# Performance work log

Hardware: AMD Instinct MI355X
Metric: run time of the kernel (lower is better)

Reference implementation:

```python
import jax, jax.numpy as jnp
import numpy as np

N_NODES = 100000
N_EDGES = 1600000
D_FEAT = 128


def setup_inputs() -> dict:
    key = jax.random.key(0)
    k1, k2 = jax.random.split(key)
    x = jax.random.normal(k1, (N_NODES, D_FEAT), dtype=jnp.float32)
    edge_index = jax.random.randint(k2, (2, N_EDGES), 0, N_NODES, dtype=jnp.int64)
    return {"x": x, "edge_index": edge_index}


def reference(x, edge_index):
    # gather source/target node features: [E, D] each
    src = x[edge_index[0]]
    dst = x[edge_index[1]]
    # per-edge dot product -> [E], then sigmoid
    dot = jnp.sum(src * dst, axis=-1)
    return jax.nn.sigmoid(dot)
```

## Files before the change

kernel.cpp:

```cpp
#include <hip/hip_runtime.h>
#include <hip/hip_fp16.h>
#include <math.h>

#define D_FEAT 128

__global__ __launch_bounds__(256) void convert_x_fp16_kernel(
    const float* __restrict__ x, __half* __restrict__ xh, int n_elems)
{
    int i = blockIdx.x * blockDim.x + threadIdx.x;
    int base = i * 8;
    if (base >= n_elems) return;
    const float4* p = reinterpret_cast<const float4*>(x + base);
    float4 f0 = p[0];
    float4 f1 = p[1];
    __half2 h[4];
    h[0] = __floats2half2_rn(f0.x, f0.y);
    h[1] = __floats2half2_rn(f0.z, f0.w);
    h[2] = __floats2half2_rn(f1.x, f1.y);
    h[3] = __floats2half2_rn(f1.z, f1.w);
    *reinterpret_cast<float4*>(xh + base) = *reinterpret_cast<float4*>(h);
}

struct alignas(16) h8 { __half2 h[4]; };

__device__ __forceinline__ float dot8(const h8& a, const h8& b) {
    float acc = 0.f;
#pragma unroll
    for (int k = 0; k < 4; ++k) {
        float2 fa = __half22float2(a.h[k]);
        float2 fb = __half22float2(b.h[k]);
        acc += fa.x * fb.x + fa.y * fb.y;
    }
    return acc;
}

__global__ __launch_bounds__(256) void edge_dot_sigmoid_fp16_kernel(
    const __half* __restrict__ xh,
    const int* __restrict__ ei,
    float* __restrict__ out,
    int n_edges)
{
    const int lane = threadIdx.x & 15;
    const int grp  = threadIdx.x >> 4;
    const int base = blockIdx.x * 32;
    const int e0 = base + grp;
    const int e1 = base + 16 + grp;

    if (e0 >= n_edges) return;

    const int s0 = ei[e0];
    const int d0 = ei[n_edges + e0];
    const bool has1 = (e1 < n_edges);
    const int s1 = has1 ? ei[e1] : s0;
    const int d1 = has1 ? ei[n_edges + e1] : d0;

    const h8* ps0 = reinterpret_cast<const h8*>(xh + (size_t)s0 * D_FEAT) + lane;
    const h8* pd0 = reinterpret_cast<const h8*>(xh + (size_t)d0 * D_FEAT) + lane;
    const h8* ps1 = reinterpret_cast<const h8*>(xh + (size_t)s1 * D_FEAT) + lane;
    const h8* pd1 = reinterpret_cast<const h8*>(xh + (size_t)d1 * D_FEAT) + lane;

    h8 a0 = *ps0;
    h8 b0 = *pd0;
    h8 a1 = *ps1;
    h8 b1 = *pd1;

    float acc0 = dot8(a0, b0);
    float acc1 = dot8(a1, b1);

    acc0 += __shfl_xor(acc0, 1, 16);
    acc0 += __shfl_xor(acc0, 2, 16);
    acc0 += __shfl_xor(acc0, 4, 16);
    acc0 += __shfl_xor(acc0, 8, 16);

    acc1 += __shfl_xor(acc1, 1, 16);
    acc1 += __shfl_xor(acc1, 2, 16);
    acc1 += __shfl_xor(acc1, 4, 16);
    acc1 += __shfl_xor(acc1, 8, 16);

    if (lane == 0) {
        out[e0] = 1.0f / (1.0f + __expf(-acc0));
        if (has1) out[e1] = 1.0f / (1.0f + __expf(-acc1));
    }
}

__global__ __launch_bounds__(256) void edge_dot_sigmoid_fp32_kernel(
    const float* __restrict__ x,
    const int* __restrict__ ei,
    float* __restrict__ out,
    int n_edges)
{
    const int lane = threadIdx.x & 15;
    const int e = blockIdx.x * 16 + (threadIdx.x >> 4);
    if (e >= n_edges) return;

    const int s = ei[e];
    const int d = ei[n_edges + e];

    const float4* sp = reinterpret_cast<const float4*>(x + (size_t)s * D_FEAT) + lane * 2;
    const float4* dp = reinterpret_cast<const float4*>(x + (size_t)d * D_FEAT) + lane * 2;

    float4 a0 = sp[0], a1 = sp[1], b0 = dp[0], b1 = dp[1];

    float acc = a0.x * b0.x + a0.y * b0.y + a0.z * b0.z + a0.w * b0.w
              + a1.x * b1.x + a1.y * b1.y + a1.z * b1.z + a1.w * b1.w;

    acc += __shfl_xor(acc, 1, 16);
    acc += __shfl_xor(acc, 2, 16);
    acc += __shfl_xor(acc, 4, 16);
    acc += __shfl_xor(acc, 8, 16);

    if (lane == 0) out[e] = 1.0f / (1.0f + __expf(-acc));
}

extern "C" void kernel_launch(void* const* d_in, const int* in_sizes, int n_in,
                              void* d_out, int out_size, void* d_ws, size_t ws_size,
                              hipStream_t stream) {
    const float* x   = (const float*)d_in[0];
    const int*   ei  = (const int*)d_in[1];
    float*       out = (float*)d_out;

    const int n_x     = in_sizes[0];
    const int n_edges = in_sizes[1] / 2;

    const size_t need = (size_t)n_x * sizeof(__half);
    if (ws_size >= need) {
        __half* xh = (__half*)d_ws;
        int n_chunks = (n_x + 7) / 8;
        convert_x_fp16_kernel<<<(n_chunks + 255) / 256, 256, 0, stream>>>(x, xh, n_x);
        dim3 grid((n_edges + 31) / 32);
        edge_dot_sigmoid_fp16_kernel<<<grid, 256, 0, stream>>>(xh, ei, out, n_edges);
    } else {
        dim3 grid((n_edges + 15) / 16);
        edge_dot_sigmoid_fp32_kernel<<<grid, 256, 0, stream>>>(x, ei, out, n_edges);
    }
}
```

Before: 111.8 us.

## Process eight edges per 16-lane group with shuffled indices and fdot2

Each 16-lane group now handles eight edges instead of two. The lanes load the source and destination indices cooperatively in one coalesced read and broadcast them with shuffles. All sixteen row gathers are issued before any arithmetic, which raises memory-level parallelism. The dot product uses the packed fp16 fdot2 builtin, and the per-edge results are gathered so that eight lanes write eight consecutive outputs. Register use rises to hold sixteen 16-byte vectors per thread, which may lower occupancy, and the grid is four times smaller.

```diff
diff --git a/kernel.cpp b/kernel.cpp
--- a/kernel.cpp
+++ b/kernel.cpp
@@ -3,6 +3,24 @@
 #include <math.h>
 
 #define D_FEAT 128
+
+typedef _Float16 f16x2 __attribute__((ext_vector_type(2)));
+struct alignas(16) h8v { f16x2 h[4]; };
+
+__device__ __forceinline__ float dot8(const h8v& a, const h8v& b, float acc) {
+#if __has_builtin(__builtin_amdgcn_fdot2)
+#pragma unroll
+    for (int k = 0; k < 4; ++k)
+        acc = __builtin_amdgcn_fdot2(a.h[k], b.h[k], acc, false);
+#else
+#pragma unroll
+    for (int k = 0; k < 4; ++k) {
+        acc += (float)a.h[k].x * (float)b.h[k].x;
+        acc += (float)a.h[k].y * (float)b.h[k].y;
+    }
+#endif
+    return acc;
+}
 
 __global__ __launch_bounds__(256) void convert_x_fp16_kernel(
     const float* __restrict__ x, __half* __restrict__ xh, int n_elems)
@@ -21,19 +39,6 @@
     *reinterpret_cast<float4*>(xh + base) = *reinterpret_cast<float4*>(h);
 }
 
-struct alignas(16) h8 { __half2 h[4]; };
-
-__device__ __forceinline__ float dot8(const h8& a, const h8& b) {
-    float acc = 0.f;
-#pragma unroll
-    for (int k = 0; k < 4; ++k) {
-        float2 fa = __half22float2(a.h[k]);
-        float2 fb = __half22float2(b.h[k]);
-        acc += fa.x * fb.x + fa.y * fb.y;
-    }
-    return acc;
-}
-
 __global__ __launch_bounds__(256) void edge_dot_sigmoid_fp16_kernel(
     const __half* __restrict__ xh,
     const int* __restrict__ ei,
@@ -42,44 +47,41 @@
 {
     const int lane = threadIdx.x & 15;
     const int grp  = threadIdx.x >> 4;
-    const int base = blockIdx.x * 32;
-    const int e0 = base + grp;
-    const int e1 = base + 16 + grp;
+    const long eb  = (long)blockIdx.x * 128 + grp * 8;
 
-    if (e0 >= n_edges) return;
+    int myidx = 0;
+    {
+        long e = eb + (lane & 7);
+        if (e < n_edges)
+            myidx = (lane < 8) ? ei[e] : ei[(long)n_edges + e];
+    }
 
-    const int s0 = ei[e0];
-    const int d0 = ei[n_edges + e0];
-    const bool has1 = (e1 < n_edges);
-    const int s1 = has1 ? ei[e1] : s0;
-    const int d1 = has1 ? ei[n_edges + e1] : d0;
+    const h8v* __restrict__ xrow = reinterpret_cast<const h8v*>(xh);
 
-    const h8* ps0 = reinterpret_cast<const h8*>(xh + (size_t)s0 * D_FEAT) + lane;
-    const h8* pd0 = reinterpret_cast<const h8*>(xh + (size_t)d0 * D_FEAT) + lane;
-    const h8* ps1 = reinterpret_cast<const h8*>(xh + (size_t)s1 * D_FEAT) + lane;
-    const h8* pd1 = reinterpret_cast<const h8*>(xh + (size_t)d1 * D_FEAT) + lane;
+    h8v a[8], b[8];
+#pragma unroll
+    for (int k = 0; k < 8; ++k) {
+        int sk = __shfl(myidx, k, 16);
+        int dk = __shfl(myidx, 8 + k, 16);
+        a[k] = xrow[(size_t)sk * 16 + lane];
+        b[k] = xrow[(size_t)dk * 16 + lane];
+    }
 
-    h8 a0 = *ps0;
-    h8 b0 = *pd0;
-    h8 a1 = *ps1;
-    h8 b1 = *pd1;
+    float r = 0.f;
+#pragma unroll
+    for (int k = 0; k < 8; ++k) {
+        float acc = dot8(a[k], b[k], 0.f);
+        acc += __shfl_xor(acc, 1, 16);
+        acc += __shfl_xor(acc, 2, 16);
+        acc += __shfl_xor(acc, 4, 16);
+        acc += __shfl_xor(acc, 8, 16);
+        if (lane == k) r = acc;
+    }
 
-    float acc0 = dot8(a0, b0);
-    float acc1 = dot8(a1, b1);
-
-    acc0 += __shfl_xor(acc0, 1, 16);
-    acc0 += __shfl_xor(acc0, 2, 16);
-    acc0 += __shfl_xor(acc0, 4, 16);
-    acc0 += __shfl_xor(acc0, 8, 16);
-
-    acc1 += __shfl_xor(acc1, 1, 16);
-    acc1 += __shfl_xor(acc1, 2, 16);
-    acc1 += __shfl_xor(acc1, 4, 16);
-    acc1 += __shfl_xor(acc1, 8, 16);
-
-    if (lane == 0) {
-        out[e0] = 1.0f / (1.0f + __expf(-acc0));
-        if (has1) out[e1] = 1.0f / (1.0f + __expf(-acc1));
+    if (lane < 8) {
+        long e = eb + lane;
+        if (e < n_edges)
+            out[e] = 1.0f / (1.0f + __expf(-r));
     }
 }
 
@@ -127,7 +129,7 @@
         __half* xh = (__half*)d_ws;
         int n_chunks = (n_x + 7) / 8;
         convert_x_fp16_kernel<<<(n_chunks + 255) / 256, 256, 0, stream>>>(x, xh, n_x);
-        dim3 grid((n_edges + 31) / 32);
+        dim3 grid((n_edges + 127) / 128);
         edge_dot_sigmoid_fp16_kernel<<<grid, 256, 0, stream>>>(xh, ei, out, n_edges);
     } else {
         dim3 grid((n_edges + 15) / 16);
```

Result: no change. 113.2 us (+1.3%).
